# Optimization experiments

Measured on AMD Instinct MI355X. Metric: run time of the kernel, lower is better.

Reference implementation:

```python
import jax, jax.numpy as jnp
import numpy as np

N_NODES = 100000
N_EDGES = 1600000
N_GRAPHS = 128
IN_FEATS = 128
OUT_FEATS = 64


def setup_inputs() -> dict:
    key = jax.random.key(0)
    k1, k2, k3, k4, k5, k6 = jax.random.split(key, 6)
    features = jax.random.normal(k1, (N_NODES, IN_FEATS), jnp.float32)
    src = jax.random.randint(k2, (N_EDGES,), 0, N_NODES, dtype=jnp.int32)
    dst = jax.random.randint(k3, (N_EDGES,), 0, N_NODES, dtype=jnp.int32)
    graph_ids = jnp.sort(jax.random.randint(k4, (N_NODES,), 0, N_GRAPHS, dtype=jnp.int32))
    # Xavier-uniform init as in DGL GraphConv
    lim1 = float(np.sqrt(6.0 / (IN_FEATS + IN_FEATS)))
    lim2 = float(np.sqrt(6.0 / (IN_FEATS + OUT_FEATS)))
    W1 = jax.random.uniform(k5, (IN_FEATS, IN_FEATS), jnp.float32, -lim1, lim1)
    W2 = jax.random.uniform(k6, (IN_FEATS, OUT_FEATS), jnp.float32, -lim2, lim2)
    b1 = jnp.zeros((IN_FEATS,), jnp.float32)
    b2 = jnp.zeros((OUT_FEATS,), jnp.float32)
    return {"features": features, "W1": W1, "b1": b1, "W2": W2, "b2": b2,
            "src": src, "dst": dst, "graph_ids": graph_ids, "num_graphs": N_GRAPHS}


def _graph_conv(x, W, b, src, dst, n_nodes):
    # DGL GraphConv, norm='both': D_dst^{-1/2} A D_src^{-1/2} X W + b
    ones = jnp.ones(src.shape, x.dtype)
    deg_out = jax.ops.segment_sum(ones, src, num_segments=n_nodes)
    deg_in = jax.ops.segment_sum(ones, dst, num_segments=n_nodes)
    norm_src = jax.lax.rsqrt(jnp.maximum(deg_out, 1.0))  # [N]
    norm_dst = jax.lax.rsqrt(jnp.maximum(deg_in, 1.0))   # [N]
    h = (x * norm_src[:, None]) @ W                       # dense transform first
    agg = jax.ops.segment_sum(h[src], dst, num_segments=n_nodes)  # spmm-style scatter-add
    return agg * norm_dst[:, None] + b


def reference(features, W1, b1, W2, b2, src, dst, graph_ids, num_graphs):
    n = features.shape[0]
    h = jax.nn.relu(_graph_conv(features, W1, b1, src, dst, n))
    h = jax.nn.relu(_graph_conv(h, W2, b2, src, dst, n))
    # dgl.mean_nodes: per-graph mean over nodes
    sums = jax.ops.segment_sum(h, graph_ids, num_segments=num_graphs)
    counts = jax.ops.segment_sum(jnp.ones((n, 1), h.dtype), graph_ids, num_segments=num_graphs)
    return sums / jnp.maximum(counts, 1.0)
```

## Files before the change

kernel.cpp:

```cpp
#include <hip/hip_runtime.h>
#include <hip/hip_bf16.h>


#define NPP_SHIFT 9
#define NPP 512
#define MAXP 256
#define NB 512

typedef __attribute__((ext_vector_type(8))) short frag8;
typedef __attribute__((ext_vector_type(4))) float f32x4;
typedef __attribute__((ext_vector_type(2))) float v2f;

__launch_bounds__(256)
__global__ void passA_count(const int* __restrict__ src, const int* __restrict__ dst,
                            int E, int P, int* __restrict__ counts_src,
                            int* __restrict__ counts_dst,
                            const int* __restrict__ gids, int N, int G,
                            int* __restrict__ gcnt) {
    __shared__ int h1[MAXP], h2[MAXP], h3[MAXP];
    int tid = threadIdx.x;
    for (int i = tid; i < MAXP; i += 256) { h1[i] = 0; h2[i] = 0; h3[i] = 0; }
    __syncthreads();
    int per_block = (E + NB - 1) / NB;
    int e0 = blockIdx.x * per_block;
    int e1 = min(e0 + per_block, E);
    for (int e = e0 + tid; e < e1; e += 256) {
        atomicAdd(&h1[src[e] >> NPP_SHIFT], 1);
        atomicAdd(&h2[dst[e] >> NPP_SHIFT], 1);
    }
    int npb = (N + NB - 1) / NB;
    int n0 = blockIdx.x * npb;
    int n1 = min(n0 + npb, N);
    for (int i = n0 + tid; i < n1; i += 256) atomicAdd(&h3[gids[i]], 1);
    __syncthreads();
    for (int i = tid; i < P; i += 256) {
        counts_src[(size_t)blockIdx.x * P + i] = h1[i];
        counts_dst[(size_t)blockIdx.x * P + i] = h2[i];
    }
    for (int i = tid; i < G; i += 256)
        if (h3[i]) atomicAdd(&gcnt[i], h3[i]);
}

__launch_bounds__(1024)
__global__ void scanB(const int* __restrict__ counts, int* __restrict__ offs,
                      int* __restrict__ ptot, int P) {
    __shared__ int s[1024];
    int tid = threadIdx.x;
    int p = blockIdx.x % P;
    int st = blockIdx.x / P;
    const int* c = counts + (size_t)st * NB * P;
    int v = (tid < NB) ? c[(size_t)tid * P + p] : 0;
    s[tid] = v;
    __syncthreads();
    for (int off = 1; off < 1024; off <<= 1) {
        int t = (tid >= off) ? s[tid - off] : 0;
        __syncthreads();
        s[tid] += t;
        __syncthreads();
    }
    if (tid < NB) offs[(size_t)st * NB * P + (size_t)tid * P + p] = s[tid] - v;
    if (tid == 1023) ptot[st * P + p] = s[1023];
}

__launch_bounds__(256)
__global__ void passC_scatter(const int* __restrict__ src, const int* __restrict__ dst,
                              int E, int P, const int* __restrict__ offs,
                              const int* __restrict__ ptot, int* __restrict__ pbase,
                              int* __restrict__ ebuf_src, int2* __restrict__ ebuf_dst) {
    __shared__ int cur1[MAXP], cur2[MAXP], sc[256];
    int tid = threadIdx.x;
    int v = (tid < P) ? ptot[tid] : 0;
    sc[tid] = v;
    __syncthreads();
    for (int off = 1; off < 256; off <<= 1) {
        int t = (tid >= off) ? sc[tid - off] : 0;
        __syncthreads();
        sc[tid] += t;
        __syncthreads();
    }
    int base0 = sc[tid] - v;
    if (tid < P) {
        cur1[tid] = base0 + offs[(size_t)blockIdx.x * P + tid];
        if (blockIdx.x == 0) pbase[tid] = base0;
    }
    __syncthreads();
    v = (tid < P) ? ptot[P + tid] : 0;
    sc[tid] = v;
    __syncthreads();
    for (int off = 1; off < 256; off <<= 1) {
        int t = (tid >= off) ? sc[tid - off] : 0;
        __syncthreads();
        sc[tid] += t;
        __syncthreads();
    }
    int base1 = sc[tid] - v;
    if (tid < P) {
        cur2[tid] = base1 + offs[(size_t)NB * P + (size_t)blockIdx.x * P + tid];
        if (blockIdx.x == 0) pbase[P + tid] = base1;
    }
    __syncthreads();
    int per_block = (E + NB - 1) / NB;
    int e0 = blockIdx.x * per_block;
    int e1 = min(e0 + per_block, E);
    for (int e = e0 + tid; e < e1; e += 256) {
        int s = src[e];
        int d = dst[e];
        int pos1 = atomicAdd(&cur1[s >> NPP_SHIFT], 1);
        ebuf_src[pos1] = s;
        int pos2 = atomicAdd(&cur2[d >> NPP_SHIFT], 1);
        ebuf_dst[pos2] = make_int2(d, s);
    }
}

__launch_bounds__(512)
__global__ void passD_build(const int* __restrict__ ebuf_src, const int2* __restrict__ ebuf_dst,
                            const int* __restrict__ ptot, const int* __restrict__ pbase,
                            float* __restrict__ norm_src, int* __restrict__ row_start,
                            int* __restrict__ csr_src, int N, int E, int P) {
    __shared__ int hs[NPP], hd[NPP], sc[NPP];
    int tid = threadIdx.x;
    int p = blockIdx.x;
    int node_lo = p << NPP_SHIFT;
    int nl = min(NPP, N - node_lo);
    hs[tid] = 0;
    hd[tid] = 0;
    __syncthreads();
    int nsrc = ptot[p];
    int base_s = pbase[p];
    for (int i = tid; i < nsrc; i += 512)
        atomicAdd(&hs[ebuf_src[base_s + i] - node_lo], 1);
    int ndst = ptot[P + p];
    int base_d = pbase[P + p];
    for (int i = tid; i < ndst; i += 512)
        atomicAdd(&hd[ebuf_dst[base_d + i].x - node_lo], 1);
    __syncthreads();
    if (tid < nl) norm_src[node_lo + tid] = rsqrtf((float)max(hs[tid], 1));
    int myh = hd[tid];
    sc[tid] = myh;
    __syncthreads();
    for (int off = 1; off < 512; off <<= 1) {
        int t = (tid >= off) ? sc[tid - off] : 0;
        __syncthreads();
        sc[tid] += t;
        __syncthreads();
    }
    int row0 = base_d + sc[tid] - myh;
    if (tid < nl) row_start[node_lo + tid] = row0;
    if (p == P - 1 && tid == 0) row_start[N] = E;
    __syncthreads();
    hd[tid] = row0;
    __syncthreads();
    for (int i = tid; i < ndst; i += 512) {
        int2 r = ebuf_dst[base_d + i];
        int pos = atomicAdd(&hd[r.x - node_lo], 1);
        csr_src[pos] = r.y;
    }
}

template <int COLS, bool BF16IN, bool PERM, bool FP8OUT>
__launch_bounds__(256)
__global__ void gemm_mfma(const void* __restrict__ xin, const float* __restrict__ w,
                          const float* __restrict__ norm,
                          void* __restrict__ out, int n) {
    constexpr int NT = COLS / 16;
    __shared__ short wlds[4 * NT * 64 * 8];
    const int tid = threadIdx.x;
    for (int i = tid; i < 128 * COLS / 4; i += 256) {
        int k = (i * 4) / COLS;
        int n0 = (i * 4) % COLS;
        float4 wv;
        if constexpr (PERM) {
            int ksrc = 64 * ((k >> 2) & 1) + 16 * (k & 3) + (k >> 3);
            wv = *reinterpret_cast<const float4*>(w + (size_t)ksrc * COLS + n0);
        } else {
            wv = reinterpret_cast<const float4*>(w)[i];
        }
        int c = k >> 5, q = (k >> 3) & 3, j = k & 7;
        float vals[4] = {wv.x, wv.y, wv.z, wv.w};
#pragma unroll
        for (int u = 0; u < 4; ++u) {
            int nn = n0 + u;
            int t = nn >> 4;
            int ln = (q << 4) | (nn & 15);
            union { __hip_bfloat16 b; short s; } cv;
            cv.b = __float2bfloat16(vals[u]);
            wlds[(((c * NT + t) << 6) | ln) * 8 + j] = cv.s;
        }
    }
    __syncthreads();

    const int lane = tid & 63;
    const int wid = tid >> 6;
    const int m = lane & 15;
    const int q = lane >> 4;
    const int ntiles = (n + 15) >> 4;
    const frag8* wfr = reinterpret_cast<const frag8*>(wlds);

    for (int wt = blockIdx.x * 4 + wid; wt < ntiles; wt += gridDim.x * 4) {
        const int row = (wt << 4) + m;
        frag8 af[4];
        if (row < n) {
            if constexpr (BF16IN) {
                const frag8* xp = reinterpret_cast<const frag8*>(
                    (const __hip_bfloat16*)xin + (size_t)row * 128);
#pragma unroll
                for (int c = 0; c < 4; ++c) af[c] = xp[c * 4 + q];
            } else {
                const float* xp = (const float*)xin + (size_t)row * 128;
                float nm = norm[row];
#pragma unroll
                for (int c = 0; c < 4; ++c) {
                    int base = c * 32 + q * 8;
                    float4 v0 = *reinterpret_cast<const float4*>(xp + base);
                    float4 v1 = *reinterpret_cast<const float4*>(xp + base + 4);
                    union { frag8 f; short s[8]; } a;
                    union { __hip_bfloat16 b; short s; } cv;
                    cv.b = __float2bfloat16(v0.x * nm); a.s[0] = cv.s;
                    cv.b = __float2bfloat16(v0.y * nm); a.s[1] = cv.s;
                    cv.b = __float2bfloat16(v0.z * nm); a.s[2] = cv.s;
                    cv.b = __float2bfloat16(v0.w * nm); a.s[3] = cv.s;
                    cv.b = __float2bfloat16(v1.x * nm); a.s[4] = cv.s;
                    cv.b = __float2bfloat16(v1.y * nm); a.s[5] = cv.s;
                    cv.b = __float2bfloat16(v1.z * nm); a.s[6] = cv.s;
                    cv.b = __float2bfloat16(v1.w * nm); a.s[7] = cv.s;
                    af[c] = a.f;
                }
            }
        } else {
#pragma unroll
            for (int c = 0; c < 4; ++c) af[c] = frag8{0, 0, 0, 0, 0, 0, 0, 0};
        }
        f32x4 acc[NT] = {};
#pragma unroll
        for (int c = 0; c < 4; ++c)
#pragma unroll
            for (int t = 0; t < NT; ++t)
                acc[t] = __builtin_amdgcn_mfma_f32_16x16x32_bf16(
                    af[c], wfr[(c * NT + t) * 64 + lane], acc[t], 0, 0, 0);
#pragma unroll
        for (int r = 0; r < 4; ++r) {
            int grow = (wt << 4) + q * 4 + r;
            if (grow < n) {
                if constexpr (FP8OUT && COLS == 128) {
                    uint w0 = 0, w1 = 0;
                    w0 = (uint)__builtin_amdgcn_cvt_pk_fp8_f32(acc[0][r], acc[1][r], (int)w0, false);
                    w0 = (uint)__builtin_amdgcn_cvt_pk_fp8_f32(acc[2][r], acc[3][r], (int)w0, true);
                    w1 = (uint)__builtin_amdgcn_cvt_pk_fp8_f32(acc[4][r], acc[5][r], (int)w1, false);
                    w1 = (uint)__builtin_amdgcn_cvt_pk_fp8_f32(acc[6][r], acc[7][r], (int)w1, true);
                    reinterpret_cast<uint2*>(out)[(size_t)grow * 16 + m] = make_uint2(w0, w1);
                } else if constexpr (FP8OUT) {
                    uint w0 = 0;
                    w0 = (uint)__builtin_amdgcn_cvt_pk_fp8_f32(acc[0][r], acc[1][r], (int)w0, false);
                    w0 = (uint)__builtin_amdgcn_cvt_pk_fp8_f32(acc[2][r], acc[3][r], (int)w0, true);
                    reinterpret_cast<uint*>(out)[(size_t)grow * 16 + m] = w0;
                } else {
                    __hip_bfloat16* ob = reinterpret_cast<__hip_bfloat16*>(out);
#pragma unroll
                    for (int t = 0; t < NT; ++t)
                        ob[(size_t)grow * COLS + t * 16 + m] = __float2bfloat16(acc[t][r]);
                }
            }
        }
    }
}

__launch_bounds__(256)
__global__ void spmm1_kernel(const uint* __restrict__ h1,
                             const int* __restrict__ row_start,
                             const int* __restrict__ csr_src,
                             const float* __restrict__ b1,
                             const float* __restrict__ norm_src,
                             uint2* __restrict__ x2n, int n) {
    int gw = (blockIdx.x * blockDim.x + threadIdx.x) >> 6;
    int lane = threadIdx.x & 63;
    if (gw >= n) return;
    int e0 = row_start[gw];
    int e1 = row_start[gw + 1];
    int a = lane >> 5;
    int s = lane & 31;
    float acc0 = 0.f, acc1 = 0.f, acc2 = 0.f, acc3 = 0.f;
    int e = e0;
    for (; e + 16 <= e1; e += 16) {
        uint v[8];
#pragma unroll
        for (int j = 0; j < 8; ++j) {
            int cs = csr_src[e + 2 * j + a];
            v[j] = h1[(size_t)cs * 32 + s];
        }
#pragma unroll
        for (int j = 0; j < 8; ++j) {
            v2f lo = __builtin_amdgcn_cvt_pk_f32_fp8((int)v[j], false);
            v2f hi = __builtin_amdgcn_cvt_pk_f32_fp8((int)v[j], true);
            acc0 += lo[0]; acc1 += lo[1]; acc2 += hi[0]; acc3 += hi[1];
        }
    }
    if (e < e1) {
        uint v[8];
#pragma unroll
        for (int j = 0; j < 8; ++j) {
            int idx = e + 2 * j + a;
            int cidx = min(idx, e1 - 1);
            int cs = csr_src[cidx];
            uint vv = h1[(size_t)cs * 32 + s];
            v[j] = (idx < e1) ? vv : 0u;
        }
#pragma unroll
        for (int j = 0; j < 8; ++j) {
            v2f lo = __builtin_amdgcn_cvt_pk_f32_fp8((int)v[j], false);
            v2f hi = __builtin_amdgcn_cvt_pk_f32_fp8((int)v[j], true);
            acc0 += lo[0]; acc1 += lo[1]; acc2 += hi[0]; acc3 += hi[1];
        }
    }
    acc0 += __shfl_xor(acc0, 32);
    acc1 += __shfl_xor(acc1, 32);
    acc2 += __shfl_xor(acc2, 32);
    acc3 += __shfl_xor(acc3, 32);
    if (a == 0) {
        float nd = rsqrtf((float)max(e1 - e0, 1));
        float ns = norm_src[gw];
        int m2 = s >> 1;
        int a2 = (s & 1) << 6;
        float f0 = fmaxf(fmaf(acc0, nd, b1[a2 + m2]), 0.f) * ns;
        float f1 = fmaxf(fmaf(acc1, nd, b1[a2 + 16 + m2]), 0.f) * ns;
        float f2 = fmaxf(fmaf(acc2, nd, b1[a2 + 32 + m2]), 0.f) * ns;
        float f3 = fmaxf(fmaf(acc3, nd, b1[a2 + 48 + m2]), 0.f) * ns;
        union { __hip_bfloat16 b; ushort u; } c0, c1, c2, c3;
        c0.b = __float2bfloat16(f0);
        c1.b = __float2bfloat16(f1);
        c2.b = __float2bfloat16(f2);
        c3.b = __float2bfloat16(f3);
        uint w0 = (uint)c0.u | ((uint)c1.u << 16);
        uint w1 = (uint)c2.u | ((uint)c3.u << 16);
        x2n[(size_t)gw * 32 + s] = make_uint2(w0, w1);
    }
}

__launch_bounds__(256)
__global__ void spmm2_kernel(const uint* __restrict__ h2,
                             const int* __restrict__ row_start,
                             const int* __restrict__ csr_src,
                             const float* __restrict__ b2,
                             const int* __restrict__ gids,
                             const int* __restrict__ gcnt,
                             float* __restrict__ out, int n) {
    int gw = (blockIdx.x * blockDim.x + threadIdx.x) >> 6;
    int lane = threadIdx.x & 63;
    int wave = threadIdx.x >> 6;
    int a = lane >> 4;
    int s = lane & 15;
    float f0 = 0.f, f1 = 0.f, f2 = 0.f, f3 = 0.f;
    int g;
    if (gw < n) {
        g = gids[gw];
        int e0 = row_start[gw];
        int e1 = row_start[gw + 1];
        float v0 = 0.f, v1 = 0.f, v2 = 0.f, v3 = 0.f;
        int e = e0;
        for (; e + 16 <= e1; e += 16) {
            uint u[4];
#pragma unroll
            for (int j = 0; j < 4; ++j)
                u[j] = h2[(size_t)csr_src[e + 4 * j + a] * 16 + s];
#pragma unroll
            for (int j = 0; j < 4; ++j) {
                v2f lo = __builtin_amdgcn_cvt_pk_f32_fp8((int)u[j], false);
                v2f hi = __builtin_amdgcn_cvt_pk_f32_fp8((int)u[j], true);
                v0 += lo[0]; v1 += lo[1]; v2 += hi[0]; v3 += hi[1];
            }
        }
        if (e < e1) {
            uint u[4];
#pragma unroll
            for (int j = 0; j < 4; ++j) {
                int idx = e + 4 * j + a;
                int cidx = min(idx, e1 - 1);
                uint vv = h2[(size_t)csr_src[cidx] * 16 + s];
                u[j] = (idx < e1) ? vv : 0u;
            }
#pragma unroll
            for (int j = 0; j < 4; ++j) {
                v2f lo = __builtin_amdgcn_cvt_pk_f32_fp8((int)u[j], false);
                v2f hi = __builtin_amdgcn_cvt_pk_f32_fp8((int)u[j], true);
                v0 += lo[0]; v1 += lo[1]; v2 += hi[0]; v3 += hi[1];
            }
        }
        v0 += __shfl_xor(v0, 16); v0 += __shfl_xor(v0, 32);
        v1 += __shfl_xor(v1, 16); v1 += __shfl_xor(v1, 32);
        v2 += __shfl_xor(v2, 16); v2 += __shfl_xor(v2, 32);
        v3 += __shfl_xor(v3, 16); v3 += __shfl_xor(v3, 32);
        float nd = rsqrtf((float)max(e1 - e0, 1));
        float inv = 1.f / (float)max(gcnt[g], 1);
        f0 = fmaxf(fmaf(v0, nd, b2[s]), 0.f) * inv;
        f1 = fmaxf(fmaf(v1, nd, b2[16 + s]), 0.f) * inv;
        f2 = fmaxf(fmaf(v2, nd, b2[32 + s]), 0.f) * inv;
        f3 = fmaxf(fmaf(v3, nd, b2[48 + s]), 0.f) * inv;
    } else {
        g = gids[n - 1];
    }
    __shared__ float sbuf[4][64];
    __shared__ int sg[4];
    if (a == 0) {
        sbuf[wave][s] = f0;
        sbuf[wave][16 + s] = f1;
        sbuf[wave][32 + s] = f2;
        sbuf[wave][48 + s] = f3;
    }
    if (lane == 0) sg[wave] = g;
    __syncthreads();
    if (wave == 0) {
        int g0 = sg[0], g1 = sg[1], g2 = sg[2], g3 = sg[3];
        if (g0 == g1 && g1 == g2 && g2 == g3) {
            float ssum = sbuf[0][lane] + sbuf[1][lane] + sbuf[2][lane] + sbuf[3][lane];
            atomicAdd(&out[(size_t)g0 * 64 + lane], ssum);
        } else {
            atomicAdd(&out[(size_t)g0 * 64 + lane], sbuf[0][lane]);
            atomicAdd(&out[(size_t)g1 * 64 + lane], sbuf[1][lane]);
            atomicAdd(&out[(size_t)g2 * 64 + lane], sbuf[2][lane]);
            atomicAdd(&out[(size_t)g3 * 64 + lane], sbuf[3][lane]);
        }
    }
}

extern "C" void kernel_launch(void* const* d_in, const int* in_sizes, int n_in,
                              void* d_out, int out_size, void* d_ws, size_t ws_size,
                              hipStream_t stream) {
    const float* features = (const float*)d_in[0];
    const float* W1 = (const float*)d_in[1];
    const float* b1 = (const float*)d_in[2];
    const float* W2 = (const float*)d_in[3];
    const float* b2 = (const float*)d_in[4];
    const int* src = (const int*)d_in[5];
    const int* dst = (const int*)d_in[6];
    const int* gids = (const int*)d_in[7];
    const int N = in_sizes[7];
    const int E = in_sizes[5];
    const int G = out_size / 64;
    float* out = (float*)d_out;
    const int P = (N + NPP - 1) >> NPP_SHIFT;

    char* ws = (char*)d_ws;
    size_t off = 0;
    auto alloc = [&](size_t bytes) -> void* {
        void* p = ws + off;
        off = (off + bytes + 255) & ~(size_t)255;
        return p;
    };
    int* counts = (int*)alloc((size_t)2 * NB * P * 4);
    int* offs = (int*)alloc((size_t)2 * NB * P * 4);
    int* ptot = (int*)alloc((size_t)2 * P * 4);
    int* pbase = (int*)alloc((size_t)2 * P * 4);
    int* gcnt = (int*)alloc((size_t)G * 4);
    int* ebuf_src = (int*)alloc((size_t)E * 4);
    int2* ebuf_dst = (int2*)alloc((size_t)E * 8);
    float* norm_src = (float*)alloc((size_t)N * 4);
    int* row_start = (int*)alloc((size_t)(N + 1) * 4);
    int* csr_src = (int*)alloc((size_t)E * 4);
    uint* h1 = (uint*)alloc((size_t)N * 128);
    __hip_bfloat16* x2n = (__hip_bfloat16*)alloc((size_t)N * 128 * 2);
    uint* h2 = h1;

    hipMemsetAsync(out, 0, (size_t)out_size * sizeof(float), stream);
    hipMemsetAsync(gcnt, 0, (size_t)G * 4, stream);

    const int B = 256;
    passA_count<<<NB, 256, 0, stream>>>(src, dst, E, P, counts, counts + (size_t)NB * P,
                                        gids, N, G, gcnt);
    scanB<<<2 * P, 1024, 0, stream>>>(counts, offs, ptot, P);
    passC_scatter<<<NB, 256, 0, stream>>>(src, dst, E, P, offs, ptot, pbase,
                                          ebuf_src, ebuf_dst);
    passD_build<<<P, 512, 0, stream>>>(ebuf_src, ebuf_dst, ptot, pbase, norm_src, row_start,
                                       csr_src, N, E, P);

    gemm_mfma<128, false, false, true><<<768, 256, 0, stream>>>(features, W1, norm_src,
                                                                (void*)h1, N);
    spmm1_kernel<<<(N * 64 + B - 1) / B, B, 0, stream>>>(h1, row_start, csr_src, b1, norm_src,
                                                         (uint2*)x2n, N);
    gemm_mfma<64, true, true, true><<<768, 256, 0, stream>>>(x2n, W2, nullptr,
                                                             (void*)h2, N);
    spmm2_kernel<<<(N * 64 + B - 1) / B, B, 0, stream>>>(h2, row_start, csr_src, b2,
                                                         gids, gcnt, out, N);
}
```

Baseline: 291.0 us.

## Process multiple destination rows per wave in both SpMM gather kernels

Each wave now handles two rows in spmm1 and four rows in spmm2, interleaving the gathers of several rows in one loop so more independent loads are in flight per wave. The grid shrinks to match. Rows of unequal degree share a loop bound set by the longest row, so some lanes do masked idle iterations. The spmm2 epilogue now pre-reduces per wave when all four rows belong to one graph and otherwise issues per-row atomics.

Result: no change. 287.9 us (-1.1%).

```diff
diff --git a/kernel.cpp b/kernel.cpp
--- a/kernel.cpp
+++ b/kernel.cpp
@@ -271,67 +271,78 @@
                              const float* __restrict__ b1,
                              const float* __restrict__ norm_src,
                              uint2* __restrict__ x2n, int n) {
-    int gw = (blockIdx.x * blockDim.x + threadIdx.x) >> 6;
+    int wv = (blockIdx.x * blockDim.x + threadIdx.x) >> 6;
     int lane = threadIdx.x & 63;
-    if (gw >= n) return;
-    int e0 = row_start[gw];
-    int e1 = row_start[gw + 1];
+    int r0 = wv * 2;
+    if (r0 >= n) return;
     int a = lane >> 5;
     int s = lane & 31;
-    float acc0 = 0.f, acc1 = 0.f, acc2 = 0.f, acc3 = 0.f;
-    int e = e0;
-    for (; e + 16 <= e1; e += 16) {
-        uint v[8];
-#pragma unroll
-        for (int j = 0; j < 8; ++j) {
-            int cs = csr_src[e + 2 * j + a];
-            v[j] = h1[(size_t)cs * 32 + s];
-        }
-#pragma unroll
-        for (int j = 0; j < 8; ++j) {
-            v2f lo = __builtin_amdgcn_cvt_pk_f32_fp8((int)v[j], false);
-            v2f hi = __builtin_amdgcn_cvt_pk_f32_fp8((int)v[j], true);
-            acc0 += lo[0]; acc1 += lo[1]; acc2 += hi[0]; acc3 += hi[1];
-        }
-    }
-    if (e < e1) {
-        uint v[8];
-#pragma unroll
-        for (int j = 0; j < 8; ++j) {
-            int idx = e + 2 * j + a;
-            int cidx = min(idx, e1 - 1);
-            int cs = csr_src[cidx];
-            uint vv = h1[(size_t)cs * 32 + s];
-            v[j] = (idx < e1) ? vv : 0u;
-        }
-#pragma unroll
-        for (int j = 0; j < 8; ++j) {
-            v2f lo = __builtin_amdgcn_cvt_pk_f32_fp8((int)v[j], false);
-            v2f hi = __builtin_amdgcn_cvt_pk_f32_fp8((int)v[j], true);
-            acc0 += lo[0]; acc1 += lo[1]; acc2 += hi[0]; acc3 += hi[1];
-        }
-    }
-    acc0 += __shfl_xor(acc0, 32);
-    acc1 += __shfl_xor(acc1, 32);
-    acc2 += __shfl_xor(acc2, 32);
-    acc3 += __shfl_xor(acc3, 32);
+    int e0[2], e1[2];
+#pragma unroll
+    for (int r = 0; r < 2; ++r) {
+        int rr = min(r0 + r, n - 1);
+        e0[r] = row_start[rr];
+        e1[r] = row_start[rr + 1];
+        if (r0 + r >= n) e1[r] = e0[r];
+    }
+    float acc[2][4] = {};
+    int nb = max((e1[0] - e0[0] + 15) >> 4, (e1[1] - e0[1] + 15) >> 4);
+    for (int b = 0; b < nb; ++b) {
+        uint v[2][8];
+#pragma unroll
+        for (int r = 0; r < 2; ++r) {
+            int base = e0[r] + b * 16;
+            if (base < e1[r]) {
+#pragma unroll
+                for (int j = 0; j < 8; ++j) {
+                    int idx = base + 2 * j + a;
+                    int cidx = min(idx, e1[r] - 1);
+                    uint vv = h1[(size_t)csr_src[cidx] * 32 + s];
+                    v[r][j] = (idx < e1[r]) ? vv : 0u;
+                }
+            } else {
+#pragma unroll
+                for (int j = 0; j < 8; ++j) v[r][j] = 0u;
+            }
+        }
+#pragma unroll
+        for (int r = 0; r < 2; ++r)
+#pragma unroll
+            for (int j = 0; j < 8; ++j) {
+                v2f lo = __builtin_amdgcn_cvt_pk_f32_fp8((int)v[r][j], false);
+                v2f hi = __builtin_amdgcn_cvt_pk_f32_fp8((int)v[r][j], true);
+                acc[r][0] += lo[0]; acc[r][1] += lo[1];
+                acc[r][2] += hi[0]; acc[r][3] += hi[1];
+            }
+    }
+#pragma unroll
+    for (int r = 0; r < 2; ++r)
+#pragma unroll
+        for (int k = 0; k < 4; ++k) acc[r][k] += __shfl_xor(acc[r][k], 32);
     if (a == 0) {
-        float nd = rsqrtf((float)max(e1 - e0, 1));
-        float ns = norm_src[gw];
         int m2 = s >> 1;
         int a2 = (s & 1) << 6;
-        float f0 = fmaxf(fmaf(acc0, nd, b1[a2 + m2]), 0.f) * ns;
-        float f1 = fmaxf(fmaf(acc1, nd, b1[a2 + 16 + m2]), 0.f) * ns;
-        float f2 = fmaxf(fmaf(acc2, nd, b1[a2 + 32 + m2]), 0.f) * ns;
-        float f3 = fmaxf(fmaf(acc3, nd, b1[a2 + 48 + m2]), 0.f) * ns;
-        union { __hip_bfloat16 b; ushort u; } c0, c1, c2, c3;
-        c0.b = __float2bfloat16(f0);
-        c1.b = __float2bfloat16(f1);
-        c2.b = __float2bfloat16(f2);
-        c3.b = __float2bfloat16(f3);
-        uint w0 = (uint)c0.u | ((uint)c1.u << 16);
-        uint w1 = (uint)c2.u | ((uint)c3.u << 16);
-        x2n[(size_t)gw * 32 + s] = make_uint2(w0, w1);
+        float bb0 = b1[a2 + m2], bb1 = b1[a2 + 16 + m2];
+        float bb2 = b1[a2 + 32 + m2], bb3 = b1[a2 + 48 + m2];
+#pragma unroll
+        for (int r = 0; r < 2; ++r) {
+            if (r0 + r < n) {
+                float nd = rsqrtf((float)max(e1[r] - e0[r], 1));
+                float ns = norm_src[r0 + r];
+                float f0 = fmaxf(fmaf(acc[r][0], nd, bb0), 0.f) * ns;
+                float f1 = fmaxf(fmaf(acc[r][1], nd, bb1), 0.f) * ns;
+                float f2 = fmaxf(fmaf(acc[r][2], nd, bb2), 0.f) * ns;
+                float f3 = fmaxf(fmaf(acc[r][3], nd, bb3), 0.f) * ns;
+                union { __hip_bfloat16 b; ushort u; } c0, c1, c2, c3;
+                c0.b = __float2bfloat16(f0);
+                c1.b = __float2bfloat16(f1);
+                c2.b = __float2bfloat16(f2);
+                c3.b = __float2bfloat16(f3);
+                uint w0 = (uint)c0.u | ((uint)c1.u << 16);
+                uint w1 = (uint)c2.u | ((uint)c3.u << 16);
+                x2n[(size_t)(r0 + r) * 32 + s] = make_uint2(w0, w1);
+            }
+        }
     }
 }
 
@@ -343,80 +354,115 @@
                              const int* __restrict__ gids,
                              const int* __restrict__ gcnt,
                              float* __restrict__ out, int n) {
-    int gw = (blockIdx.x * blockDim.x + threadIdx.x) >> 6;
+    int wv = (blockIdx.x * blockDim.x + threadIdx.x) >> 6;
     int lane = threadIdx.x & 63;
     int wave = threadIdx.x >> 6;
+    int r0 = wv * 4;
     int a = lane >> 4;
     int s = lane & 15;
-    float f0 = 0.f, f1 = 0.f, f2 = 0.f, f3 = 0.f;
-    int g;
-    if (gw < n) {
-        g = gids[gw];
-        int e0 = row_start[gw];
-        int e1 = row_start[gw + 1];
-        float v0 = 0.f, v1 = 0.f, v2 = 0.f, v3 = 0.f;
-        int e = e0;
-        for (; e + 16 <= e1; e += 16) {
-            uint u[4];
-#pragma unroll
-            for (int j = 0; j < 4; ++j)
-                u[j] = h2[(size_t)csr_src[e + 4 * j + a] * 16 + s];
+    int e0[4], e1[4], g[4];
+    float inv[4];
+#pragma unroll
+    for (int r = 0; r < 4; ++r) {
+        int rr = min(r0 + r, n - 1);
+        e0[r] = row_start[rr];
+        e1[r] = row_start[rr + 1];
+        g[r] = gids[rr];
+        if (r0 + r >= n) { e1[r] = e0[r]; g[r] = -1; }
+        inv[r] = 1.f / (float)max(gcnt[max(g[r], 0)], 1);
+    }
+    float acc[4][4] = {};
+    int nb = 0;
+#pragma unroll
+    for (int r = 0; r < 4; ++r) nb = max(nb, (e1[r] - e0[r] + 15) >> 4);
+    for (int b = 0; b < nb; ++b) {
+        uint u[4][4];
+#pragma unroll
+        for (int r = 0; r < 4; ++r) {
+            int base = e0[r] + b * 16;
+            if (base < e1[r]) {
+#pragma unroll
+                for (int j = 0; j < 4; ++j) {
+                    int idx = base + 4 * j + a;
+                    int cidx = min(idx, e1[r] - 1);
+                    uint vv = h2[(size_t)csr_src[cidx] * 16 + s];
+                    u[r][j] = (idx < e1[r]) ? vv : 0u;
+                }
+            } else {
+#pragma unroll
+                for (int j = 0; j < 4; ++j) u[r][j] = 0u;
+            }
+        }
+#pragma unroll
+        for (int r = 0; r < 4; ++r)
 #pragma unroll
             for (int j = 0; j < 4; ++j) {
-                v2f lo = __builtin_amdgcn_cvt_pk_f32_fp8((int)u[j], false);
-                v2f hi = __builtin_amdgcn_cvt_pk_f32_fp8((int)u[j], true);
-                v0 += lo[0]; v1 += lo[1]; v2 += hi[0]; v3 += hi[1];
-            }
-        }
-        if (e < e1) {
-            uint u[4];
-#pragma unroll
-            for (int j = 0; j < 4; ++j) {
-                int idx = e + 4 * j + a;
-                int cidx = min(idx, e1 - 1);
-                uint vv = h2[(size_t)csr_src[cidx] * 16 + s];
-                u[j] = (idx < e1) ? vv : 0u;
-            }
-#pragma unroll
-            for (int j = 0; j < 4; ++j) {
-                v2f lo = __builtin_amdgcn_cvt_pk_f32_fp8((int)u[j], false);
-                v2f hi = __builtin_amdgcn_cvt_pk_f32_fp8((int)u[j], true);
-                v0 += lo[0]; v1 += lo[1]; v2 += hi[0]; v3 += hi[1];
-            }
-        }
-        v0 += __shfl_xor(v0, 16); v0 += __shfl_xor(v0, 32);
-        v1 += __shfl_xor(v1, 16); v1 += __shfl_xor(v1, 32);
-        v2 += __shfl_xor(v2, 16); v2 += __shfl_xor(v2, 32);
-        v3 += __shfl_xor(v3, 16); v3 += __shfl_xor(v3, 32);
-        float nd = rsqrtf((float)max(e1 - e0, 1));
-        float inv = 1.f / (float)max(gcnt[g], 1);
-        f0 = fmaxf(fmaf(v0, nd, b2[s]), 0.f) * inv;
-        f1 = fmaxf(fmaf(v1, nd, b2[16 + s]), 0.f) * inv;
-        f2 = fmaxf(fmaf(v2, nd, b2[32 + s]), 0.f) * inv;
-        f3 = fmaxf(fmaf(v3, nd, b2[48 + s]), 0.f) * inv;
-    } else {
-        g = gids[n - 1];
+                v2f lo = __builtin_amdgcn_cvt_pk_f32_fp8((int)u[r][j], false);
+                v2f hi = __builtin_amdgcn_cvt_pk_f32_fp8((int)u[r][j], true);
+                acc[r][0] += lo[0]; acc[r][1] += lo[1];
+                acc[r][2] += hi[0]; acc[r][3] += hi[1];
+            }
+    }
+#pragma unroll
+    for (int r = 0; r < 4; ++r)
+#pragma unroll
+        for (int k = 0; k < 4; ++k) {
+            acc[r][k] += __shfl_xor(acc[r][k], 16);
+            acc[r][k] += __shfl_xor(acc[r][k], 32);
+        }
+    float bb0 = b2[s], bb1 = b2[16 + s], bb2v = b2[32 + s], bb3 = b2[48 + s];
+    float val[4][4];
+#pragma unroll
+    for (int r = 0; r < 4; ++r) {
+        float nd = rsqrtf((float)max(e1[r] - e0[r], 1));
+        bool vld = g[r] >= 0;
+        val[r][0] = vld ? fmaxf(fmaf(acc[r][0], nd, bb0), 0.f) * inv[r] : 0.f;
+        val[r][1] = vld ? fmaxf(fmaf(acc[r][1], nd, bb1), 0.f) * inv[r] : 0.f;
+        val[r][2] = vld ? fmaxf(fmaf(acc[r][2], nd, bb2v), 0.f) * inv[r] : 0.f;
+        val[r][3] = vld ? fmaxf(fmaf(acc[r][3], nd, bb3), 0.f) * inv[r] : 0.f;
     }
     __shared__ float sbuf[4][64];
     __shared__ int sg[4];
-    if (a == 0) {
-        sbuf[wave][s] = f0;
-        sbuf[wave][16 + s] = f1;
-        sbuf[wave][32 + s] = f2;
-        sbuf[wave][48 + s] = f3;
-    }
-    if (lane == 0) sg[wave] = g;
+    bool same = (g[0] == g[1]) && (g[1] == g[2]) && (g[2] == g[3]) && (g[0] >= 0);
+    int sgw;
+    if (same) {
+        if (a == 0) {
+            sbuf[wave][s]      = val[0][0] + val[1][0] + val[2][0] + val[3][0];
+            sbuf[wave][16 + s] = val[0][1] + val[1][1] + val[2][1] + val[3][1];
+            sbuf[wave][32 + s] = val[0][2] + val[1][2] + val[2][2] + val[3][2];
+            sbuf[wave][48 + s] = val[0][3] + val[1][3] + val[2][3] + val[3][3];
+        }
+        sgw = g[0];
+    } else {
+        if (a == 0) {
+#pragma unroll
+            for (int r = 0; r < 4; ++r) {
+                if (g[r] >= 0) {
+                    atomicAdd(&out[(size_t)g[r] * 64 + s], val[r][0]);
+                    atomicAdd(&out[(size_t)g[r] * 64 + 16 + s], val[r][1]);
+                    atomicAdd(&out[(size_t)g[r] * 64 + 32 + s], val[r][2]);
+                    atomicAdd(&out[(size_t)g[r] * 64 + 48 + s], val[r][3]);
+                }
+            }
+            sbuf[wave][s] = 0.f;
+            sbuf[wave][16 + s] = 0.f;
+            sbuf[wave][32 + s] = 0.f;
+            sbuf[wave][48 + s] = 0.f;
+        }
+        sgw = -1;
+    }
+    if (lane == 0) sg[wave] = sgw;
     __syncthreads();
     if (wave == 0) {
         int g0 = sg[0], g1 = sg[1], g2 = sg[2], g3 = sg[3];
-        if (g0 == g1 && g1 == g2 && g2 == g3) {
+        if (g0 == g1 && g1 == g2 && g2 == g3 && g0 >= 0) {
             float ssum = sbuf[0][lane] + sbuf[1][lane] + sbuf[2][lane] + sbuf[3][lane];
             atomicAdd(&out[(size_t)g0 * 64 + lane], ssum);
         } else {
-            atomicAdd(&out[(size_t)g0 * 64 + lane], sbuf[0][lane]);
-            atomicAdd(&out[(size_t)g1 * 64 + lane], sbuf[1][lane]);
-            atomicAdd(&out[(size_t)g2 * 64 + lane], sbuf[2][lane]);
-            atomicAdd(&out[(size_t)g3 * 64 + lane], sbuf[3][lane]);
+#pragma unroll
+            for (int w = 0; w < 4; ++w)
+                if (sg[w] >= 0)
+                    atomicAdd(&out[(size_t)sg[w] * 64 + lane], sbuf[w][lane]);
         }
     }
 }
@@ -462,7 +508,6 @@
     hipMemsetAsync(out, 0, (size_t)out_size * sizeof(float), stream);
     hipMemsetAsync(gcnt, 0, (size_t)G * 4, stream);
 
-    const int B = 256;
     passA_count<<<NB, 256, 0, stream>>>(src, dst, E, P, counts, counts + (size_t)NB * P,
                                         gids, N, G, gcnt);
     scanB<<<2 * P, 1024, 0, stream>>>(counts, offs, ptot, P);
@@ -473,10 +518,18 @@
 
     gemm_mfma<128, false, false, true><<<768, 256, 0, stream>>>(features, W1, norm_src,
                                                                 (void*)h1, N);
-    spmm1_kernel<<<(N * 64 + B - 1) / B, B, 0, stream>>>(h1, row_start, csr_src, b1, norm_src,
-                                                         (uint2*)x2n, N);
+    {
+        int waves = (N + 1) / 2;
+        int blocks = (waves * 64 + 255) / 256;
+        spmm1_kernel<<<blocks, 256, 0, stream>>>(h1, row_start, csr_src, b1, norm_src,
+                                                 (uint2*)x2n, N);
+    }
     gemm_mfma<64, true, true, true><<<768, 256, 0, stream>>>(x2n, W2, nullptr,
                                                              (void*)h2, N);
-    spmm2_kernel<<<(N * 64 + B - 1) / B, B, 0, stream>>>(h2, row_start, csr_src, b2,
-                                                         gids, gcnt, out, N);
-}
+    {
+        int waves = (N + 3) / 4;
+        int blocks = (waves * 64 + 255) / 256;
+        spmm2_kernel<<<blocks, 256, 0, stream>>>(h2, row_start, csr_src, b2,
+                                                 gids, gcnt, out, N);
+    }
+}
```
